# Kernel optimization log

Hardware: AMD Instinct MI355X
Metric: run time of the kernel (lower is better)

The kernel has to match this reference:

```python
import jax, jax.numpy as jnp
import numpy as np

N, D, V = 4096, 256, 32000
B, T = 32, 256
U_DECAY, X_DECAY = 0.97, 0.97
EPS = 1e-6


def layernorm_row(z):
    # matches torch: (z - mean) / (std + eps), std with Bessel correction (ddof=1)
    m = jnp.mean(z, axis=-1, keepdims=True)
    s = jnp.std(z, axis=-1, keepdims=True, ddof=1)
    return (z - m) / (s + EPS)


def setup_inputs() -> dict:
    key = jax.random.key(0)
    k1, k2, k3, k4, k5 = jax.random.split(key, 5)
    token_emb = jax.random.normal(k1, (V, D), jnp.float32) / np.float32(np.sqrt(D))
    E = jax.random.normal(k2, (D, N), jnp.float32) / np.float32(np.sqrt(N))
    Dx = jax.random.normal(k3, (N, D), jnp.float32) / np.float32(np.sqrt(D))
    Dy = jax.random.normal(k4, (N, D), jnp.float32) / np.float32(np.sqrt(D))
    idx = jax.random.randint(k5, (B, T), 0, V)
    return {"idx": idx, "token_emb": token_emb, "E": E, "Dx": Dx, "Dy": Dy}


def reference(idx, token_emb, E, Dx, Dy):
    b = idx.shape[0]

    def step(carry, tok):
        x, rho = carry                                   # x: (b,n), rho: (b,d,n)
        v_prev = token_emb[tok]                          # (b,d) embedding gather
        x_t = X_DECAY * x + jax.nn.relu(v_prev @ Dx.T)   # (b,n)
        x_t = x_t / (jnp.sum(jnp.abs(x_t), axis=-1, keepdims=True) + EPS)  # L1 normalize
        a_star = jnp.einsum('bdn,bn->bd', rho, x_t)      # fast-weight readout
        y_t = jax.nn.relu(layernorm_row(a_star) @ Dy.T) * jax.nn.relu(x_t)  # (b,n)
        v_star = layernorm_row(y_t @ E.T)                # (b,d)
        # Hebbian decayed outer-product memory update
        rho = U_DECAY * (rho + jnp.einsum('bd,bn->bdn', layernorm_row(v_prev), x_t))
        return (x_t, rho), v_star

    x0 = jnp.zeros((b, N), jnp.float32)
    rho0 = jnp.zeros((b, D, N), jnp.float32)
    (_, _), vs = jax.lax.scan(step, (x0, rho0), idx.T)   # vs: (T,b,d)
    return jnp.transpose(vs, (1, 0, 2))                  # (b,T,d)
```

## Files before the change

### kernel.cpp

```cpp
#include <hip/hip_runtime.h>
#include <hip/hip_bf16.h>

#define NN 4096
#define DD 256
#define BB 32
#define TT 256
#define EPS 1e-6f
#define DECAY 0.97f
#define LOG2_DECAY -0.043943348f

typedef __hip_bfloat16 bf16;
typedef short short8 __attribute__((ext_vector_type(8)));
typedef float floatx4 __attribute__((ext_vector_type(4)));

__device__ __forceinline__ float bfu2f(short u) {
    return __uint_as_float(((unsigned)(unsigned short)u) << 16);
}

__device__ __forceinline__ short f2bfu(float f) {
    bf16 t = __float2bfloat16(f);
    return *reinterpret_cast<short*>(&t);
}

__device__ __forceinline__ float blk_sum_256(float v, volatile float* s4) {
#pragma unroll
    for (int o = 32; o > 0; o >>= 1) v += __shfl_down(v, o, 64);
    int lane = threadIdx.x & 63, w = threadIdx.x >> 6;
    __syncthreads();
    if (lane == 0) s4[w] = v;
    __syncthreads();
    return s4[0] + s4[1] + s4[2] + s4[3];
}

__device__ __forceinline__ void gl16(const bf16* g, bf16* l) {
    __builtin_amdgcn_global_load_lds((const __attribute__((address_space(1))) void*)g,
                                     (__attribute__((address_space(3))) void*)l, 16, 0, 0);
}

__global__ void k_detect(const unsigned short* __restrict__ raw, int* __restrict__ flag) {
    __shared__ int cnt[4];
    int tid = threadIdx.x;
    int bad = 0;
    for (int i = tid; i < 8192; i += 256) {
        unsigned int u = raw[2 * i];
        float v = __uint_as_float(u << 16);
        if (!(fabsf(v) < 1e6f)) bad++;
    }
#pragma unroll
    for (int o = 32; o > 0; o >>= 1) bad += __shfl_down(bad, o, 64);
    int lane = tid & 63, w = tid >> 6;
    if (lane == 0) cnt[w] = bad;
    __syncthreads();
    if (tid == 0) flag[0] = (cnt[0] + cnt[1] + cnt[2] + cnt[3] < 32) ? 1 : 0;
}

__global__ __launch_bounds__(256) void k_convert3(const void* __restrict__ s0,
                                                  const void* __restrict__ s1,
                                                  const void* __restrict__ s2,
                                                  bf16* __restrict__ d0,
                                                  bf16* __restrict__ d1,
                                                  bf16* __restrict__ d2,
                                                  const int* __restrict__ flag) {
    const int per = NN * DD / 8;
    int i = blockIdx.x * 256 + threadIdx.x;
    int m = i / per, j = i % per;
    const void* s = (m == 0) ? s0 : (m == 1) ? s1 : s2;
    bf16* d = (m == 0) ? d0 : (m == 1) ? d1 : d2;
    if (flag[0]) {
        ((uint4*)d)[j] = ((const uint4*)s)[j];
    } else {
        const float4* f = (const float4*)s;
        float4 a = f[2 * j], b = f[2 * j + 1];
        short8 o;
        float va[8] = {a.x, a.y, a.z, a.w, b.x, b.y, b.z, b.w};
#pragma unroll
        for (int k = 0; k < 8; k++) o[k] = f2bfu(va[k]);
        ((short8*)d)[j] = o;
    }
}

__global__ __launch_bounds__(256) void k_gather_ln(const void* __restrict__ emb,
                                                   const int* __restrict__ idx,
                                                   bf16* __restrict__ Vpb,
                                                   bf16* __restrict__ Ub,
                                                   const int* __restrict__ flag) {
    __shared__ float s4[4];
    int r = blockIdx.x, d = threadIdx.x;
    int tok = idx[r];
    long o = (long)tok * DD + d;
    float e = flag[0] ? __bfloat162float(((const bf16*)emb)[o]) : ((const float*)emb)[o];
    Vpb[(long)r * DD + d] = __float2bfloat16(e);
    float m = blk_sum_256(e, s4) * (1.0f / DD);
    float zc = e - m;
    float var = blk_sum_256(zc * zc, s4) * (1.0f / (DD - 1));
    Ub[(long)r * DD + d] = __float2bfloat16(zc / (sqrtf(fmaxf(var, 0.f)) + EPS));
}

__global__ __launch_bounds__(256) void k_transpose(const bf16* __restrict__ Ub,
                                                   bf16* __restrict__ Ut) {
    __shared__ bf16 tile[32][33];
    int b = blockIdx.z;
    int t0 = blockIdx.x * 32, d0 = blockIdx.y * 32;
    const bf16* src = Ub + (long)b * TT * DD;
    bf16* dst = Ut + (long)b * DD * TT;
    int rr = threadIdx.x >> 3, c4 = (threadIdx.x & 7) * 4;
#pragma unroll
    for (int i = 0; i < 4; i++) tile[rr][c4 + i] = src[(long)(t0 + rr) * DD + d0 + c4 + i];
    __syncthreads();
#pragma unroll
    for (int i = 0; i < 4; i++) dst[(long)(d0 + rr) * TT + t0 + c4 + i] = tile[c4 + i][rr];
}

enum { EPI_RELU_BF16 = 0, EPI_NONE_F32 = 1, EPI_RELU_MULX_BF16 = 2, EPI_NONE_BF16 = 3,
       EPI_MASK_BF16 = 4 };

template <int EPI>
__global__ __launch_bounds__(512, 2) void k_fused256(const bf16* __restrict__ A,
                                                     const bf16* __restrict__ B,
                                                     bf16* __restrict__ C,
                                                     const bf16* __restrict__ Xaux,
                                                     float* __restrict__ Wsum) {
    __shared__ __align__(16) char smem[65536];
    bf16* R = (bf16*)smem;

    int bx = blockIdx.x, by = blockIdx.y;
    {
        int gx = gridDim.x;
        int nwg = gx * gridDim.y;
        int id = by * gx + bx;
        int q = nwg >> 3;
        int nid = (id & 7) * q + (id >> 3);
        bx = nid % gx;
        by = nid / gx;
    }
    int bm = by * 256, bn = bx * 256;
    int tid = threadIdx.x, wid = tid >> 6, lane = tid & 63;
    int wr = wid >> 2, wc = wid & 3;
    int lm = lane & 15, kh = lane >> 4;

    int srow2 = tid >> 2;
    int swzcol = (((tid & 3) ^ ((srow2 >> 1) & 3)) << 3);
    const bf16* gA0 = A + (long)(bm + srow2) * DD + swzcol;
    const bf16* gA1 = gA0 + (long)128 * DD;
    const bf16* gB0 = B + (long)(bn + srow2) * DD + swzcol;
    const bf16* gB1 = gB0 + (long)128 * DD;
    int chunk = ((kh ^ ((lm >> 1) & 3)) << 3);

    floatx4 acc[8][4];
#pragma unroll
    for (int i = 0; i < 8; i++)
#pragma unroll
        for (int j = 0; j < 4; j++) acc[i][j] = (floatx4){0.f, 0.f, 0.f, 0.f};

#define STAGE256(SBASE, KK)                             \
    {                                                   \
        bf16* As_ = (bf16*)(SBASE);                     \
        bf16* Bs_ = As_ + 8192;                         \
        gl16(gA0 + (KK), As_ + tid * 8);                \
        gl16(gA1 + (KK), As_ + 4096 + tid * 8);         \
        gl16(gB0 + (KK), Bs_ + tid * 8);                \
        gl16(gB1 + (KK), Bs_ + 4096 + tid * 8);         \
    }

    STAGE256(smem, 0);

    int cur = 0;
#pragma unroll
    for (int k0 = 0; k0 < 256; k0 += 32) {
        __builtin_amdgcn_s_barrier();
        __builtin_amdgcn_sched_barrier(0);
        if (k0 + 32 < 256) STAGE256(smem + ((cur ^ 1) * 32768), k0 + 32);
        if (k0 + 32 < 256) asm volatile("s_waitcnt vmcnt(4)" ::: "memory");
        else               asm volatile("s_waitcnt vmcnt(0)" ::: "memory");
        __builtin_amdgcn_s_barrier();
        __builtin_amdgcn_sched_barrier(0);
        bf16* cbA = (bf16*)(smem + cur * 32768);
        bf16* cbB = cbA + 8192;
        short8 af[8], bfr[4];
#pragma unroll
        for (int i = 0; i < 8; i++)
            af[i] = *(const short8*)(cbA + (wr * 128 + i * 16 + lm) * 32 + chunk);
#pragma unroll
        for (int j = 0; j < 4; j++)
            bfr[j] = *(const short8*)(cbB + (wc * 64 + j * 16 + lm) * 32 + chunk);
#pragma unroll
        for (int i = 0; i < 8; i++)
#pragma unroll
            for (int j = 0; j < 4; j++)
                acc[i][j] = __builtin_amdgcn_mfma_f32_16x16x32_bf16(af[i], bfr[j], acc[i][j], 0, 0, 0);
        cur ^= 1;
    }
#undef STAGE256

#pragma unroll
    for (int p = 0; p < 4; p++) {
        __syncthreads();
        if (wr == (p >> 1)) {
            int ibase = (p & 1) * 4;
#pragma unroll
            for (int ii = 0; ii < 4; ii++)
#pragma unroll
                for (int j = 0; j < 4; j++)
#pragma unroll
                    for (int r = 0; r < 4; r++) {
                        int rr = ii * 16 + kh * 4 + r;
                        int cc = wc * 64 + j * 16 + lm;
                        R[rr * 264 + cc] = __float2bfloat16(fmaxf(acc[ibase + ii][j][r], 0.f));
                    }
        }
        __syncthreads();
#pragma unroll
        for (int it = 0; it < 4; it++) {
            int row_l = it * 16 + (tid >> 5);
            int c8 = (tid & 31) * 8;
            short8 vv = *(const short8*)(R + row_l * 264 + c8);
            int gm = bm + p * 64 + row_l;
            long off = (long)gm * NN + bn + c8;
            if (EPI == EPI_RELU_BF16) {
                *(short8*)(C + off) = vv;
                float s = 0.f;
#pragma unroll
                for (int k = 0; k < 8; k++) s += bfu2f(vv[k]);
#pragma unroll
                for (int o = 16; o > 0; o >>= 1) s += __shfl_down(s, o, 32);
                if ((tid & 31) == 0) atomicAdd(&Wsum[gm], s);
            } else {
                short8 xx = *(const short8*)(Xaux + off);
                short8 oo;
#pragma unroll
                for (int k = 0; k < 8; k++) {
                    float prod = bfu2f(vv[k]) * fmaxf(bfu2f(xx[k]), 0.f);
                    oo[k] = f2bfu(prod);
                }
                *(short8*)(C + off) = oo;
            }
        }
    }
}

template <int EPI, int KSPLIT, int TRI, int SWZ>
__global__ __launch_bounds__(256) void k_mfma_nt(int K,
                                                 const bf16* __restrict__ A, int lda, long sA,
                                                 const bf16* __restrict__ B, int ldb, long sB,
                                                 void* __restrict__ Cv, int ldc, long sC,
                                                 const bf16* __restrict__ Xaux,
                                                 float* __restrict__ Wsum) {
    __shared__ __align__(16) char smem[49152];
    bf16* R = (bf16*)smem;

    int z = blockIdx.z;
    int bz = z / KSPLIT, ks = z % KSPLIT;
    A += (long)bz * sA;
    B += (long)bz * sB;
    int bx = blockIdx.x, by = blockIdx.y;
    if (TRI) {
        by = (blockIdx.x >= 1) ? 1 : 0;
        bx = (blockIdx.x == 2) ? 1 : 0;
    }
    if (SWZ) {
        int gx = gridDim.x;
        int nwg = gx * gridDim.y;
        int id = by * gx + bx;
        int q = nwg >> 3;
        int nid = (id & 7) * q + (id >> 3);
        bx = nid % gx;
        by = nid / gx;
    }
    int bm = by * 128, bn = bx * 128;
    int tid = threadIdx.x;
    int srow = tid >> 2;
    int scol = ((((srow >> 1) & 3) ^ (tid & 3)) << 3);
    int w = tid >> 6, lane = tid & 63;
    int wm = (w >> 1) * 64, wn = (w & 1) * 64;
    int lm = lane & 15, kh = lane >> 4;

    floatx4 acc[4][4];
#pragma unroll
    for (int i = 0; i < 4; i++)
#pragma unroll
        for (int j = 0; j < 4; j++) acc[i][j] = (floatx4){0.f, 0.f, 0.f, 0.f};

    int kchunk = K / KSPLIT;
    int kbeg = ks * kchunk, kend = kbeg + kchunk;
    const bf16* gA0 = A + (long)(bm + srow) * lda + scol;
    const bf16* gA1 = gA0 + (long)64 * lda;
    const bf16* gB0 = B + (long)(bn + srow) * ldb + scol;
    const bf16* gB1 = gB0 + (long)64 * ldb;
    int dslot = tid * 8;

#define STAGE_SLOT(SBASE, KK)                          \
    {                                                  \
        bf16* bufA = (bf16*)(SBASE);                   \
        bf16* bufB = bufA + 4096;                      \
        gl16(gA0 + (KK), bufA + dslot);                \
        gl16(gA1 + (KK), bufA + 2048 + dslot);         \
        gl16(gB0 + (KK), bufB + dslot);                \
        gl16(gB1 + (KK), bufB + 2048 + dslot);         \
    }

    STAGE_SLOT(smem, kbeg);
    if (kbeg + 32 < kend) STAGE_SLOT(smem + 16384, kbeg + 32);

    int cur = 0;
    for (int k0 = kbeg; k0 < kend; k0 += 32) {
        __builtin_amdgcn_s_barrier();
        __builtin_amdgcn_sched_barrier(0);
        if (k0 + 64 < kend) {
            int ps = (cur == 0) ? 2 : cur - 1;
            STAGE_SLOT(smem + ps * 16384, k0 + 64);
        }
        int rem = (kend - k0 - 32) >> 5;
        if (rem >= 2)      asm volatile("s_waitcnt vmcnt(8)" ::: "memory");
        else if (rem == 1) asm volatile("s_waitcnt vmcnt(4)" ::: "memory");
        else               asm volatile("s_waitcnt vmcnt(0)" ::: "memory");
        __builtin_amdgcn_s_barrier();
        __builtin_amdgcn_sched_barrier(0);
        bf16* cbA = (bf16*)(smem + cur * 16384);
        bf16* cbB = cbA + 4096;
        short8 af[4], bfr[4];
#pragma unroll
        for (int i = 0; i < 4; i++) {
            int row = wm + i * 16 + lm;
            af[i] = *(const short8*)(cbA + row * 32 + ((((row >> 1) & 3) ^ kh) << 3));
        }
#pragma unroll
        for (int j = 0; j < 4; j++) {
            int row = wn + j * 16 + lm;
            bfr[j] = *(const short8*)(cbB + row * 32 + ((((row >> 1) & 3) ^ kh) << 3));
        }
#pragma unroll
        for (int i = 0; i < 4; i++)
#pragma unroll
            for (int j = 0; j < 4; j++)
                acc[i][j] = __builtin_amdgcn_mfma_f32_16x16x32_bf16(af[i], bfr[j], acc[i][j], 0, 0, 0);
        cur = (cur == 2) ? 0 : cur + 1;
    }
#undef STAGE_SLOT

    if (EPI == EPI_NONE_F32) {
        long cbase = (long)z * sC;
#pragma unroll
        for (int i = 0; i < 4; i++)
#pragma unroll
            for (int j = 0; j < 4; j++)
#pragma unroll
                for (int r = 0; r < 4; r++) {
                    int gm = bm + wm + i * 16 + kh * 4 + r;
                    int gn = bn + wn + j * 16 + lm;
                    ((float*)Cv)[cbase + (long)gm * ldc + gn] = acc[i][j][r];
                }
        return;
    }

    bf16* Cb = (bf16*)Cv + (long)z * sC;
#pragma unroll
    for (int p = 0; p < 2; p++) {
        __syncthreads();
        if ((w >> 1) == p) {
#pragma unroll
            for (int i = 0; i < 4; i++)
#pragma unroll
                for (int j = 0; j < 4; j++)
#pragma unroll
                    for (int r = 0; r < 4; r++) {
                        int rr = i * 16 + kh * 4 + r;
                        int cc = wn + j * 16 + lm;
                        float val = acc[i][j][r];
                        if (EPI == EPI_RELU_BF16 || EPI == EPI_RELU_MULX_BF16) val = fmaxf(val, 0.f);
                        R[rr * 136 + cc] = __float2bfloat16(val);
                    }
        }
        __syncthreads();
#pragma unroll
        for (int it = 0; it < 4; it++) {
            int row_l = it * 16 + (tid >> 4);
            int c8 = (tid & 15) * 8;
            short8 vv = *(const short8*)(R + row_l * 136 + c8);
            int gm = bm + p * 64 + row_l;
            long off = (long)gm * ldc + bn + c8;
            if (EPI == EPI_NONE_BF16) {
                *(short8*)(Cb + off) = vv;
            } else if (EPI == EPI_MASK_BF16) {
                short8 oo;
#pragma unroll
                for (int k = 0; k < 8; k++) {
                    int s = bn + c8 + k;
                    float f = bfu2f(vv[k]);
                    f = (s < gm) ? f * exp2f((float)(gm - s) * LOG2_DECAY) : 0.f;
                    oo[k] = f2bfu(f);
                }
                *(short8*)(Cb + off) = oo;
            } else if (EPI == EPI_RELU_BF16) {
                *(short8*)(Cb + off) = vv;
                float s = 0.f;
#pragma unroll
                for (int k = 0; k < 8; k++) s += bfu2f(vv[k]);
#pragma unroll
                for (int o = 8; o > 0; o >>= 1) s += __shfl_down(s, o, 16);
                if ((tid & 15) == 0) atomicAdd(&Wsum[gm], s);
            } else {
                short8 xx = *(const short8*)(Xaux + off);
                short8 oo;
#pragma unroll
                for (int k = 0; k < 8; k++) {
                    float prod = bfu2f(vv[k]) * fmaxf(bfu2f(xx[k]), 0.f);
                    oo[k] = f2bfu(prod);
                }
                *(short8*)(Cb + off) = oo;
            }
        }
    }
}

__global__ __launch_bounds__(256) void k_astar(const bf16* __restrict__ Gp,
                                               const bf16* __restrict__ Ut,
                                               bf16* __restrict__ Ap) {
    __shared__ __align__(16) char smem[32768];
    bf16* R = (bf16*)smem;

    int b = blockIdx.z;
    int y = blockIdx.y;
    int by = (y >= 1) ? 1 : 0, ks = (y == 2) ? 1 : 0;
    int bx = blockIdx.x;
    int bm = by * 128, bn = bx * 128, kbeg = ks * 128;
    int tid = threadIdx.x;
    int srow = tid >> 2;
    int scol = ((((srow >> 1) & 3) ^ (tid & 3)) << 3);
    int w = tid >> 6, lane = tid & 63;
    int wm = (w >> 1) * 64, wn = (w & 1) * 64;
    int lm = lane & 15, kh = lane >> 4;

    const bf16* gA = Gp + (long)b * 4 * 65536;
    long aoff0 = (long)(bm + srow) * TT + scol + kbeg;
    long aoff1 = (long)(bm + srow + 64) * TT + scol + kbeg;
    const bf16* gB0 = Ut + (long)b * DD * TT + (long)(bn + srow) * TT + scol + kbeg;
    const bf16* gB1 = gB0 + (long)64 * TT;
    int dslot = tid * 8;

    floatx4 acc[4][4];
#pragma unroll
    for (int i = 0; i < 4; i++)
#pragma unroll
        for (int j = 0; j < 4; j++) acc[i][j] = (floatx4){0.f, 0.f, 0.f, 0.f};

#define LOAD4SUM(DST, AOFF)                                        \
    {                                                              \
        short8 p0 = *(const short8*)(gA + (AOFF));                 \
        short8 p1 = *(const short8*)(gA + 65536 + (AOFF));         \
        short8 p2 = *(const short8*)(gA + 2 * 65536 + (AOFF));     \
        short8 p3 = *(const short8*)(gA + 3 * 65536 + (AOFF));     \
        short8 o_;                                                 \
        _Pragma("unroll")                                          \
        for (int k_ = 0; k_ < 8; k_++)                             \
            o_[k_] = f2bfu(bfu2f(p0[k_]) + bfu2f(p1[k_]) +         \
                           bfu2f(p2[k_]) + bfu2f(p3[k_]));         \
        DST = o_;                                                  \
    }

    {
        bf16* As_ = (bf16*)smem;
        bf16* Bs_ = As_ + 4096;
        gl16(gB0, Bs_ + dslot);
        gl16(gB1, Bs_ + 2048 + dslot);
        short8 ra0, ra1;
        LOAD4SUM(ra0, aoff0);
        LOAD4SUM(ra1, aoff1);
        *(short8*)(As_ + dslot) = ra0;
        *(short8*)(As_ + 2048 + dslot) = ra1;
    }
    __syncthreads();

    int cur = 0;
    for (int kk = 0; kk < 128; kk += 32) {
        bf16* cbA = (bf16*)(smem + cur * 16384);
        bf16* cbB = cbA + 4096;
        bf16* nbA = (bf16*)(smem + (cur ^ 1) * 16384);
        bf16* nbB = nbA + 4096;
        short8 na0, na1;
        bool has = (kk + 32) < 128;
        if (has) {
            gl16(gB0 + kk + 32, nbB + dslot);
            gl16(gB1 + kk + 32, nbB + 2048 + dslot);
            LOAD4SUM(na0, aoff0 + kk + 32);
            LOAD4SUM(na1, aoff1 + kk + 32);
        }
        short8 af[4], bfr[4];
#pragma unroll
        for (int i = 0; i < 4; i++) {
            int row = wm + i * 16 + lm;
            af[i] = *(const short8*)(cbA + row * 32 + ((((row >> 1) & 3) ^ kh) << 3));
        }
#pragma unroll
        for (int j = 0; j < 4; j++) {
            int row = wn + j * 16 + lm;
            bfr[j] = *(const short8*)(cbB + row * 32 + ((((row >> 1) & 3) ^ kh) << 3));
        }
#pragma unroll
        for (int i = 0; i < 4; i++)
#pragma unroll
            for (int j = 0; j < 4; j++)
                acc[i][j] = __builtin_amdgcn_mfma_f32_16x16x32_bf16(af[i], bfr[j], acc[i][j], 0, 0, 0);
        if (has) {
            *(short8*)(nbA + dslot) = na0;
            *(short8*)(nbA + 2048 + dslot) = na1;
        }
        __syncthreads();
        cur ^= 1;
    }
#undef LOAD4SUM

    bf16* Cb = Ap + ((long)b * 2 + ks) * 65536;
#pragma unroll
    for (int p = 0; p < 2; p++) {
        __syncthreads();
        if ((w >> 1) == p) {
#pragma unroll
            for (int i = 0; i < 4; i++)
#pragma unroll
                for (int j = 0; j < 4; j++)
#pragma unroll
                    for (int r = 0; r < 4; r++) {
                        int rr = i * 16 + kh * 4 + r;
                        int cc = wn + j * 16 + lm;
                        R[rr * 136 + cc] = __float2bfloat16(acc[i][j][r]);
                    }
        }
        __syncthreads();
#pragma unroll
        for (int it = 0; it < 4; it++) {
            int row_l = it * 16 + (tid >> 4);
            int c8 = (tid & 15) * 8;
            short8 vv = *(const short8*)(R + row_l * 136 + c8);
            int gm = bm + p * 64 + row_l;
            *(short8*)(Cb + (long)gm * DD + bn + c8) = vv;
        }
    }
}

__global__ __launch_bounds__(256) void k_scalar_scan(const float* __restrict__ Wsum,
                                                     float* __restrict__ invS) {
    __shared__ float sw[BB * TT];
    for (int i = threadIdx.x; i < BB * TT; i += 256) sw[i] = Wsum[i];
    __syncthreads();
    int b = threadIdx.x;
    if (b < BB) {
        float sig = 0.f;
        for (int t = 0; t < TT; t++) {
            float S = DECAY * sig + sw[b * TT + t];
            float inv = 1.f / (S + EPS);
            invS[b * TT + t] = inv;
            sig = S * inv;
        }
    }
}

__global__ __launch_bounds__(256) void k_colscan(bf16* __restrict__ W,
                                                 const float* __restrict__ invS) {
    __shared__ float sv[TT];
    int b = blockIdx.y;
    sv[threadIdx.x] = invS[b * TT + threadIdx.x];
    __syncthreads();
    int n = blockIdx.x * 256 + threadIdx.x;
    bf16* p = W + (long)b * TT * NN + n;
    float x = 0.f;
    for (int t = 0; t < TT; t++) {
        float w = __bfloat162float(p[(long)t * NN]);
        x = (DECAY * x + w) * sv[t];
        p[(long)t * NN] = __float2bfloat16(x);
    }
}

__global__ __launch_bounds__(256) void k_ln_rows(const bf16* __restrict__ Ap,
                                                 bf16* __restrict__ O) {
    __shared__ float s4[4];
    long r = blockIdx.x;
    int d = threadIdx.x;
    long b = r >> 8, t = r & 255;
    long base = (b * 2) * 65536 + t * 256 + d;
    float z = bfu2f(*(const short*)&Ap[base]);
    if (t >= 128) z += bfu2f(*(const short*)&Ap[base + 65536]);
    float m = blk_sum_256(z, s4) * (1.0f / DD);
    float zc = z - m;
    float var = blk_sum_256(zc * zc, s4) * (1.0f / (DD - 1));
    O[r * DD + d] = __float2bfloat16(zc / (sqrtf(fmaxf(var, 0.f)) + EPS));
}

__global__ __launch_bounds__(256) void k_final_ln(const float* __restrict__ Zp,
                                                  void* __restrict__ out,
                                                  const int* __restrict__ flag) {
    __shared__ float s4[4];
    long r = blockIdx.x;
    int d = threadIdx.x;
    const long SL = (long)8192 * 256;
    long o = r * DD + d;
    float z = Zp[o] + Zp[o + SL];
    float m = blk_sum_256(z, s4) * (1.0f / DD);
    float zc = z - m;
    float var = blk_sum_256(zc * zc, s4) * (1.0f / (DD - 1));
    float v = zc / (sqrtf(fmaxf(var, 0.f)) + EPS);
    if (flag[0]) ((bf16*)out)[o] = __float2bfloat16(v);
    else ((float*)out)[o] = v;
}

extern "C" void kernel_launch(void* const* d_in, const int* in_sizes, int n_in,
                              void* d_out, int out_size, void* d_ws, size_t ws_size,
                              hipStream_t stream) {
    const int* idx = (const int*)d_in[0];
    const void* emb = d_in[1];
    const void* E = d_in[2];
    const void* Dx = d_in[3];
    const void* Dy = d_in[4];

    char* base = (char*)d_ws;
    size_t off = 0;
    int* flag = (int*)base; off += 1024;
    bf16* Dxb = (bf16*)(base + off); off += (size_t)NN * DD * 2;
    bf16* Dyb = (bf16*)(base + off); off += (size_t)NN * DD * 2;
    bf16* Eb  = (bf16*)(base + off); off += (size_t)DD * NN * 2;
    bf16* Vpb = (bf16*)(base + off); off += (size_t)BB * TT * DD * 2;
    bf16* Ub  = (bf16*)(base + off); off += (size_t)BB * TT * DD * 2;
    bf16* Ut  = (bf16*)(base + off); off += (size_t)BB * TT * DD * 2;
    float* Wsum = (float*)(base + off); off += (size_t)BB * TT * 4;
    float* invS = (float*)(base + off); off += (size_t)BB * TT * 4;
    bf16* ALNb = (bf16*)(base + off); off += (size_t)BB * TT * DD * 2;
    bf16* Gp = (bf16*)(base + off); off += (size_t)4 * BB * TT * TT * 2;
    bf16* Ap = (bf16*)(base + off); off += (size_t)2 * BB * TT * DD * 2;
    float* Zp = (float*)Gp;
    bf16* Xb = (bf16*)(base + off); off += (size_t)BB * TT * NN * 2;

    const int M = BB * TT;

    k_detect<<<1, 256, 0, stream>>>((const unsigned short*)emb, flag);
    k_convert3<<<3 * NN * DD / 8 / 256, 256, 0, stream>>>(Dx, Dy, E, Dxb, Dyb, Eb, flag);
    k_gather_ln<<<M, 256, 0, stream>>>(emb, idx, Vpb, Ub, flag);
    k_transpose<<<dim3(8, 8, BB), 256, 0, stream>>>(Ub, Ut);

    hipMemsetAsync(Wsum, 0, (size_t)M * 4, stream);

    k_fused256<EPI_RELU_BF16><<<dim3(16, 32), 512, 0, stream>>>(Vpb, Dxb, Xb, nullptr, Wsum);

    k_scalar_scan<<<1, 256, 0, stream>>>(Wsum, invS);
    k_colscan<<<dim3(16, BB, 1), 256, 0, stream>>>(Xb, invS);

    k_mfma_nt<EPI_MASK_BF16, 4, 1, 0><<<dim3(3, 1, BB * 4), 256, 0, stream>>>(
        NN, Xb, NN, (long)TT * NN, Xb, NN, (long)TT * NN, Gp, TT, (long)TT * TT, nullptr, nullptr);

    k_astar<<<dim3(2, 3, BB), 256, 0, stream>>>(Gp, Ut, Ap);
    k_ln_rows<<<M, 256, 0, stream>>>(Ap, ALNb);

    k_fused256<EPI_RELU_MULX_BF16><<<dim3(16, 32), 512, 0, stream>>>(ALNb, Dyb, Xb, Xb, nullptr);

    k_mfma_nt<EPI_NONE_F32, 2, 0, 1><<<dim3(2, 64, 2), 256, 0, stream>>>(
        NN, Xb, NN, 0, Eb, NN, 0, Zp, DD, (long)M * DD, nullptr, nullptr);

    k_final_ln<<<M, 256, 0, stream>>>(Zp, d_out, flag);
}
```

Baseline: 321.3 us.

## Add dedicated split-K bf16 GEMM for output projection and vectorize column scan

```diff
diff --git a/kernel.cpp b/kernel.cpp
--- a/kernel.cpp
+++ b/kernel.cpp
@@ -412,6 +412,105 @@
     }
 }
 
+__global__ __launch_bounds__(512, 2) void k_zgemm(const bf16* __restrict__ A,
+                                                  const bf16* __restrict__ B,
+                                                  bf16* __restrict__ Zp) {
+    __shared__ __align__(16) char smem[49152];
+    bf16* R = (bf16*)smem;
+
+    int bx = blockIdx.x;
+    {
+        int nid = (bx & 7) * 8 + (bx >> 3);
+        bx = nid;
+    }
+    int ks = blockIdx.y;
+    int bm = bx * 128;
+    int kbeg = ks * 1024, kend = kbeg + 1024;
+
+    int tid = threadIdx.x, wid = tid >> 6, lane = tid & 63;
+    int wr = wid >> 2, wc = wid & 3;
+    int lm = lane & 15, kh = lane >> 4;
+
+    int srow = tid >> 2;
+    int swzcol = (((tid & 3) ^ ((srow >> 1) & 3)) << 3);
+    const bf16* gA  = A + (long)(bm + srow) * NN + swzcol;
+    const bf16* gB0 = B + (long)srow * NN + swzcol;
+    const bf16* gB1 = gB0 + (long)128 * NN;
+    int chunk = ((kh ^ ((lm >> 1) & 3)) << 3);
+
+    floatx4 acc[4][4];
+#pragma unroll
+    for (int i = 0; i < 4; i++)
+#pragma unroll
+        for (int j = 0; j < 4; j++) acc[i][j] = (floatx4){0.f, 0.f, 0.f, 0.f};
+
+#define STAGEZ(SBASE, KK)                               \
+    {                                                   \
+        bf16* As_ = (bf16*)(SBASE);                     \
+        bf16* Bs_ = As_ + 4096;                         \
+        gl16(gA + (KK), As_ + tid * 8);                 \
+        gl16(gB0 + (KK), Bs_ + tid * 8);                \
+        gl16(gB1 + (KK), Bs_ + 4096 + tid * 8);         \
+    }
+
+    STAGEZ(smem, kbeg);
+
+    int cur = 0;
+    for (int k0 = kbeg; k0 < kend; k0 += 32) {
+        __builtin_amdgcn_s_barrier();
+        __builtin_amdgcn_sched_barrier(0);
+        bool has = (k0 + 32) < kend;
+        if (has) STAGEZ(smem + ((cur ^ 1) * 24576), k0 + 32);
+        if (has) asm volatile("s_waitcnt vmcnt(3)" ::: "memory");
+        else     asm volatile("s_waitcnt vmcnt(0)" ::: "memory");
+        __builtin_amdgcn_s_barrier();
+        __builtin_amdgcn_sched_barrier(0);
+        bf16* cbA = (bf16*)(smem + cur * 24576);
+        bf16* cbB = cbA + 4096;
+        short8 af[4], bfr[4];
+#pragma unroll
+        for (int i = 0; i < 4; i++)
+            af[i] = *(const short8*)(cbA + (wr * 64 + i * 16 + lm) * 32 + chunk);
+#pragma unroll
+        for (int j = 0; j < 4; j++)
+            bfr[j] = *(const short8*)(cbB + (wc * 64 + j * 16 + lm) * 32 + chunk);
+#pragma unroll
+        for (int i = 0; i < 4; i++)
+#pragma unroll
+            for (int j = 0; j < 4; j++)
+                acc[i][j] = __builtin_amdgcn_mfma_f32_16x16x32_bf16(af[i], bfr[j], acc[i][j], 0, 0, 0);
+        cur ^= 1;
+    }
+#undef STAGEZ
+
+    bf16* Cb = Zp + (long)ks * 8192 * DD;
+#pragma unroll
+    for (int p = 0; p < 2; p++) {
+        __syncthreads();
+        if (wr == p) {
+#pragma unroll
+            for (int i = 0; i < 4; i++)
+#pragma unroll
+                for (int j = 0; j < 4; j++)
+#pragma unroll
+                    for (int r = 0; r < 4; r++) {
+                        int rr = i * 16 + kh * 4 + r;
+                        int cc = wc * 64 + j * 16 + lm;
+                        R[rr * 264 + cc] = __float2bfloat16(acc[i][j][r]);
+                    }
+        }
+        __syncthreads();
+#pragma unroll
+        for (int it = 0; it < 4; it++) {
+            int row_l = it * 16 + (tid >> 5);
+            int c8 = (tid & 31) * 8;
+            short8 vv = *(const short8*)(R + row_l * 264 + c8);
+            int gm = bm + p * 64 + row_l;
+            *(short8*)(Cb + (long)gm * DD + c8) = vv;
+        }
+    }
+}
+
 __global__ __launch_bounds__(256) void k_astar(const bf16* __restrict__ Gp,
                                                const bf16* __restrict__ Ut,
                                                bf16* __restrict__ Ap) {
@@ -560,13 +659,24 @@
     int b = blockIdx.y;
     sv[threadIdx.x] = invS[b * TT + threadIdx.x];
     __syncthreads();
-    int n = blockIdx.x * 256 + threadIdx.x;
-    bf16* p = W + (long)b * TT * NN + n;
-    float x = 0.f;
+    int n4 = blockIdx.x * 256 + threadIdx.x;
+    uint2* p = (uint2*)(W + (long)b * TT * NN) + n4;
+    const int STR = NN / 4;
+    float x0 = 0.f, x1 = 0.f, x2 = 0.f, x3 = 0.f;
+    uint2 cur = p[0];
     for (int t = 0; t < TT; t++) {
-        float w = __bfloat162float(p[(long)t * NN]);
-        x = (DECAY * x + w) * sv[t];
-        p[(long)t * NN] = __float2bfloat16(x);
+        uint2 nxt;
+        if (t + 1 < TT) nxt = p[(t + 1) * STR];
+        float s = sv[t];
+        x0 = (DECAY * x0 + bfu2f((short)(cur.x & 0xffff))) * s;
+        x1 = (DECAY * x1 + bfu2f((short)(cur.x >> 16))) * s;
+        x2 = (DECAY * x2 + bfu2f((short)(cur.y & 0xffff))) * s;
+        x3 = (DECAY * x3 + bfu2f((short)(cur.y >> 16))) * s;
+        uint2 o;
+        o.x = (unsigned)(unsigned short)f2bfu(x0) | ((unsigned)(unsigned short)f2bfu(x1) << 16);
+        o.y = (unsigned)(unsigned short)f2bfu(x2) | ((unsigned)(unsigned short)f2bfu(x3) << 16);
+        p[t * STR] = o;
+        cur = nxt;
     }
 }
 
@@ -585,7 +695,7 @@
     O[r * DD + d] = __float2bfloat16(zc / (sqrtf(fmaxf(var, 0.f)) + EPS));
 }
 
-__global__ __launch_bounds__(256) void k_final_ln(const float* __restrict__ Zp,
+__global__ __launch_bounds__(256) void k_final_ln(const bf16* __restrict__ Zp,
                                                   void* __restrict__ out,
                                                   const int* __restrict__ flag) {
     __shared__ float s4[4];
@@ -593,7 +703,8 @@
     int d = threadIdx.x;
     const long SL = (long)8192 * 256;
     long o = r * DD + d;
-    float z = Zp[o] + Zp[o + SL];
+    float z = bfu2f(*(const short*)&Zp[o]) + bfu2f(*(const short*)&Zp[o + SL]) +
+              bfu2f(*(const short*)&Zp[o + 2 * SL]) + bfu2f(*(const short*)&Zp[o + 3 * SL]);
     float m = blk_sum_256(z, s4) * (1.0f / DD);
     float zc = z - m;
     float var = blk_sum_256(zc * zc, s4) * (1.0f / (DD - 1));
@@ -625,7 +736,7 @@
     bf16* ALNb = (bf16*)(base + off); off += (size_t)BB * TT * DD * 2;
     bf16* Gp = (bf16*)(base + off); off += (size_t)4 * BB * TT * TT * 2;
     bf16* Ap = (bf16*)(base + off); off += (size_t)2 * BB * TT * DD * 2;
-    float* Zp = (float*)Gp;
+    bf16* Zp = Gp;
     bf16* Xb = (bf16*)(base + off); off += (size_t)BB * TT * NN * 2;
 
     const int M = BB * TT;
@@ -640,7 +751,7 @@
     k_fused256<EPI_RELU_BF16><<<dim3(16, 32), 512, 0, stream>>>(Vpb, Dxb, Xb, nullptr, Wsum);
 
     k_scalar_scan<<<1, 256, 0, stream>>>(Wsum, invS);
-    k_colscan<<<dim3(16, BB, 1), 256, 0, stream>>>(Xb, invS);
+    k_colscan<<<dim3(4, BB, 1), 256, 0, stream>>>(Xb, invS);
 
     k_mfma_nt<EPI_MASK_BF16, 4, 1, 0><<<dim3(3, 1, BB * 4), 256, 0, stream>>>(
         NN, Xb, NN, (long)TT * NN, Xb, NN, (long)TT * NN, Gp, TT, (long)TT * TT, nullptr, nullptr);
@@ -650,8 +761,7 @@
 
     k_fused256<EPI_RELU_MULX_BF16><<<dim3(16, 32), 512, 0, stream>>>(ALNb, Dyb, Xb, Xb, nullptr);
 
-    k_mfma_nt<EPI_NONE_F32, 2, 0, 1><<<dim3(2, 64, 2), 256, 0, stream>>>(
-        NN, Xb, NN, 0, Eb, NN, 0, Zp, DD, (long)M * DD, nullptr, nullptr);
+    k_zgemm<<<dim3(64, 4), 512, 0, stream>>>(Xb, Eb, Zp);
 
     k_final_ln<<<M, 256, 0, stream>>>(Zp, d_out, flag);
 }
```

Result: slower. 351.9 us (+9.5%).
